# Performance work log

Measured on AMD Instinct MI355X. Metric: run time of the kernel, lower is better.

## Reference

```python
import jax, jax.numpy as jnp
import numpy as np

B, D = 4096, 512
BASE_TAU = 0.02
CLAMP_MAX = 1e36


def _l2norm(x, eps=1e-12):
    # torch F.normalize(p=2): x / max(||x||, eps)
    n = jnp.sqrt(jnp.sum(x * x, axis=-1, keepdims=True))
    return x / jnp.maximum(n, eps)


def setup_inputs() -> dict:
    key = jax.random.key(0)
    k1, k2, k3, k4, k5, k6 = jax.random.split(key, 6)
    return {
        "visual_feats": jax.random.normal(k1, (B, D), dtype=jnp.float32),
        "textual_feats": jax.random.normal(k2, (B, D), dtype=jnp.float32),
        "pid": jax.random.randint(k3, (B,), 0, 1024, dtype=jnp.int64 if jax.config.jax_enable_x64 else jnp.int32),
        "adaptive_margins": jax.random.uniform(k4, (B,), dtype=jnp.float32),
        "uncertainty_scores": jax.random.uniform(k5, (B,), dtype=jnp.float32),
        "sample_types": jax.random.randint(k6, (B,), 0, 3, dtype=jnp.int64 if jax.config.jax_enable_x64 else jnp.int32),
    }


def reference(visual_feats, textual_feats, pid, adaptive_margins, uncertainty_scores, sample_types):
    tau = BASE_TAU
    vn = _l2norm(visual_feats)
    tn = _l2norm(textual_feats)
    scores = tn @ vn.T  # [B, B]

    # Faithful to the original loop: every iteration i builds a [B,B] matrix
    # whose rows are all scores[i,:] and uses the FULL pid vector, then takes
    # row 0 of the per-sample loss. So the label/mask row is always pid[0]'s.
    labels0 = (pid == pid[0]).astype(scores.dtype)  # [B]
    mask0 = 1.0 - labels0                            # [B]
    n_neg0 = jnp.sum(mask0)

    margins = jax.lax.stop_gradient(adaptive_margins)  # .item() in torch -> no grad

    e = jnp.exp(scores / tau)  # [B, B]
    # i2t branch (row 0 of expanded matrix == scores[i,:], mask row = mask0)
    alpha = jax.lax.stop_gradient(e * labels0 / jnp.sum(e * labels0, axis=1, keepdims=True))  # [B,B]
    neg_sum = jnp.minimum(jnp.sum(e * mask0, axis=1), CLAMP_MAX)  # [B]
    loss_i2t = jnp.maximum(-jnp.sum(alpha * scores, axis=1) + tau * jnp.log(neg_sum) + margins, 0.0)

    # t2i branch: row 0 of expanded.T is scores[i,0] repeated B times;
    # alpha_t2i row 0 sums to 1 so -(alpha*s).sum == -scores[i,0].
    s0 = scores[:, 0]  # [B]
    t2i_sum = jnp.minimum(jnp.exp(s0 / tau) * n_neg0, CLAMP_MAX)
    loss_t2i = jnp.maximum(-s0 + tau * jnp.log(t2i_sum) + margins, 0.0)

    per_sample_losses = loss_i2t + loss_t2i  # [B]

    uncertain = sample_types == 2
    uncertainty_weights = jnp.where(
        uncertain,
        jnp.clip(1.0 - 0.5 * uncertainty_scores, 0.1, 1.0),
        jnp.ones_like(uncertainty_scores),
    )
    final_loss = jnp.sum(per_sample_losses * uncertainty_weights) / jnp.sum(uncertainty_weights)
    return final_loss, per_sample_losses, uncertainty_weights, scores
```

## Files before the change

### kernel.cpp

```cpp
#include <hip/hip_runtime.h>
#include <hip/hip_bf16.h>
#include <stdint.h>

#define NB 4096
#define ND 512
#define TAU_ 0.02f
#define INV_TAU_ 50.0f
#define CLAMP_MAXF 1e36f

typedef __attribute__((ext_vector_type(8))) short bf16x8;
typedef __attribute__((ext_vector_type(4))) float f32x4;

#define AS1(p) ((__attribute__((address_space(1))) void*)(uintptr_t)(p))
#define AS3(p) ((__attribute__((address_space(3))) void*)(uint32_t)(uintptr_t)(p))

static __device__ __forceinline__ unsigned short f2bf(float f) {
  __hip_bfloat16 h = __float2bfloat16(f);
  return *reinterpret_cast<unsigned short*>(&h);
}

__global__ __launch_bounds__(256) void k_norm(const float* __restrict__ vis,
                                              const float* __restrict__ txt,
                                              const int* __restrict__ pid,
                                              unsigned short* __restrict__ tn_b,
                                              unsigned short* __restrict__ vn_b,
                                              float* __restrict__ nneg) {
  if (blockIdx.x == 2048) {
    __shared__ float r4[4];
    int tid = threadIdx.x;
    int pid0 = pid[0];
    float c = 0.f;
    for (int j = tid; j < NB; j += 256) c += (pid[j] != pid0) ? 1.0f : 0.0f;
#pragma unroll
    for (int o = 32; o; o >>= 1) c += __shfl_xor(c, o, 64);
    if ((tid & 63) == 0) r4[tid >> 6] = c;
    __syncthreads();
    if (tid == 0) nneg[0] = r4[0] + r4[1] + r4[2] + r4[3];
    return;
  }
  int wv = threadIdx.x >> 6, ln = threadIdx.x & 63;
  int r = blockIdx.x * 4 + wv;
  const float* src;
  unsigned short* dst;
  if (r < NB) {
    src = txt + (size_t)r * ND;
    dst = tn_b + (size_t)r * ND;
  } else {
    src = vis + (size_t)(r - NB) * ND;
    dst = vn_b + (size_t)(r - NB) * ND;
  }
  float4 x0 = reinterpret_cast<const float4*>(src)[ln];
  float4 x1 = reinterpret_cast<const float4*>(src)[64 + ln];
  float ss = x0.x * x0.x + x0.y * x0.y + x0.z * x0.z + x0.w * x0.w +
             x1.x * x1.x + x1.y * x1.y + x1.z * x1.z + x1.w * x1.w;
#pragma unroll
  for (int o = 32; o; o >>= 1) ss += __shfl_xor(ss, o, 64);
  float inv = 1.0f / fmaxf(sqrtf(ss), 1e-12f);
  ushort4 p0, p1;
  p0.x = f2bf(x0.x * inv); p0.y = f2bf(x0.y * inv);
  p0.z = f2bf(x0.z * inv); p0.w = f2bf(x0.w * inv);
  p1.x = f2bf(x1.x * inv); p1.y = f2bf(x1.y * inv);
  p1.z = f2bf(x1.z * inv); p1.w = f2bf(x1.w * inv);
  reinterpret_cast<ushort4*>(dst)[ln] = p0;
  reinterpret_cast<ushort4*>(dst)[64 + ln] = p1;
}

__global__ __launch_bounds__(512, 2) void k_gemm(const unsigned short* __restrict__ A,
                                                 const unsigned short* __restrict__ Bm,
                                                 const int* __restrict__ pid,
                                                 float* __restrict__ C,
                                                 float* __restrict__ partials) {
  __shared__ unsigned short smem[4][2][256 * 32];
  int tid = threadIdx.x;
  int wv = tid >> 6, ln = tid & 63;
  int tile = (blockIdx.x & 7) * 32 + (blockIdx.x >> 3);
  int bm = tile >> 4;
  int bn = tile & 15;
  int wr = wv >> 2, wc = wv & 3;
  int frow = ln & 15, fkg = ln >> 4;
  f32x4 acc[8][4] = {};
  const unsigned short* Abase = A + (size_t)(bm * 256) * ND;
  const unsigned short* Bbase = Bm + (size_t)(bn * 256) * ND;

#define STAGE(bidx, k0)                                                         \
  {                                                                             \
    _Pragma("unroll") for (int p = 0; p < 2; ++p) {                             \
      int s = p * 512 + tid;                                                    \
      int rr = s >> 2;                                                          \
      int sg = ((s & 3) + (rr >> 1)) & 3;                                       \
      __builtin_amdgcn_global_load_lds(                                         \
          AS1(Abase + (size_t)rr * ND + (k0) + sg * 8),                         \
          AS3((char*)&smem[bidx][0][0] + (p * 512 + wv * 64) * 16), 16, 0, 0);  \
      __builtin_amdgcn_global_load_lds(                                         \
          AS1(Bbase + (size_t)rr * ND + (k0) + sg * 8),                         \
          AS3((char*)&smem[bidx][1][0] + (p * 512 + wv * 64) * 16), 16, 0, 0);  \
    }                                                                           \
  }

#define COMPUTE(bidx)                                                           \
  {                                                                             \
    const char* pA = (const char*)&smem[bidx][0][0];                            \
    const char* pB = (const char*)&smem[bidx][1][0];                            \
    bf16x8 af[8], bfr[4];                                                       \
    _Pragma("unroll") for (int mi = 0; mi < 8; ++mi) {                          \
      int row = wr * 128 + mi * 16 + frow;                                      \
      af[mi] = *reinterpret_cast<const bf16x8*>(                                \
          pA + row * 64 + (((fkg - (row >> 1)) & 3) * 16));                     \
    }                                                                           \
    _Pragma("unroll") for (int ni = 0; ni < 4; ++ni) {                          \
      int row = wc * 64 + ni * 16 + frow;                                       \
      bfr[ni] = *reinterpret_cast<const bf16x8*>(                               \
          pB + row * 64 + (((fkg - (row >> 1)) & 3) * 16));                     \
    }                                                                           \
    __builtin_amdgcn_s_setprio(1);                                              \
    _Pragma("unroll") for (int mi = 0; mi < 8; ++mi)                            \
      _Pragma("unroll") for (int ni = 0; ni < 4; ++ni)                          \
        acc[mi][ni] = __builtin_amdgcn_mfma_f32_16x16x32_bf16(af[mi], bfr[ni],  \
                                                              acc[mi][ni], 0, 0, 0); \
    __builtin_amdgcn_s_setprio(0);                                              \
  }

  STAGE(0, 0);
  STAGE(1, 32);
  for (int t = 0; t < 15; ++t) {
    asm volatile("s_waitcnt vmcnt(4)" ::: "memory");
    __builtin_amdgcn_s_barrier();
    if (t < 14) STAGE((t + 2) & 3, (t + 2) * 32);
    COMPUTE(t & 3);
  }
  asm volatile("s_waitcnt vmcnt(0)" ::: "memory");
  __builtin_amdgcn_s_barrier();
  COMPUTE(3);

  int pid0 = pid[0];
  int eq[4];
#pragma unroll
  for (int ni = 0; ni < 4; ++ni)
    eq[ni] = (pid[bn * 256 + wc * 64 + ni * 16 + frow] == pid0) ? 1 : 0;

  float* pb = reinterpret_cast<float*>(&smem[0][0][0]);
  float* Cp = C + (size_t)(bm * 256 + wr * 128 + fkg * 4) * NB + bn * 256 +
              wc * 64 + frow;
#pragma unroll
  for (int mi = 0; mi < 8; ++mi) {
#pragma unroll
    for (int v = 0; v < 4; ++v) {
      float sp = 0.f, sn = 0.f, sa = 0.f;
      float* rp = Cp + (size_t)(mi * 16 + v) * NB;
#pragma unroll
      for (int ni = 0; ni < 4; ++ni) {
        float s = acc[mi][ni][v];
        rp[ni * 16] = s;
        float e = __expf(s * INV_TAU_);
        if (eq[ni]) {
          sp += e;
          sa += e * s;
        } else {
          sn += e;
        }
      }
#pragma unroll
      for (int o = 1; o < 16; o <<= 1) {
        sp += __shfl_xor(sp, o, 64);
        sn += __shfl_xor(sn, o, 64);
        sa += __shfl_xor(sa, o, 64);
      }
      if (frow == 0) {
        int row = wr * 128 + mi * 16 + fkg * 4 + v;
        pb[(wc * 256 + row) * 3 + 0] = sp;
        pb[(wc * 256 + row) * 3 + 1] = sn;
        pb[(wc * 256 + row) * 3 + 2] = sa;
      }
    }
  }
  __syncthreads();
  if (tid < 256) {
    float sp = 0.f, sn = 0.f, sa = 0.f;
#pragma unroll
    for (int w = 0; w < 4; ++w) {
      sp += pb[(w * 256 + tid) * 3 + 0];
      sn += pb[(w * 256 + tid) * 3 + 1];
      sa += pb[(w * 256 + tid) * 3 + 2];
    }
    float* pout = partials + ((size_t)(bm * 256 + tid) * 16 + bn) * 3;
    pout[0] = sp;
    pout[1] = sn;
    pout[2] = sa;
  }
}

__global__ __launch_bounds__(256) void k_row2(const float* __restrict__ partials,
                                              const float* __restrict__ scores,
                                              const float* __restrict__ margins,
                                              const float* __restrict__ unc,
                                              const int* __restrict__ stypes,
                                              const float* __restrict__ nneg,
                                              float* __restrict__ psl,
                                              float* __restrict__ uw) {
  int wv = threadIdx.x >> 6, ln = threadIdx.x & 63;
  int row = blockIdx.x * 4 + wv;
  const float* p = partials + (size_t)row * 16 * 3;
  float sp = 0.f, sn = 0.f, sa = 0.f;
  if (ln < 16) {
    sp = p[ln * 3 + 0];
    sn = p[ln * 3 + 1];
    sa = p[ln * 3 + 2];
  }
#pragma unroll
  for (int o = 1; o < 16; o <<= 1) {
    sp += __shfl_xor(sp, o, 64);
    sn += __shfl_xor(sn, o, 64);
    sa += __shfl_xor(sa, o, 64);
  }
  if (ln == 0) {
    float s0v = scores[(size_t)row * NB];
    float m = margins[row];
    float li2t = fmaxf(-(sa / sp) + TAU_ * logf(fminf(sn, CLAMP_MAXF)) + m, 0.f);
    float t2i = fminf(__expf(s0v * INV_TAU_) * nneg[0], CLAMP_MAXF);
    float lt2i = fmaxf(-s0v + TAU_ * logf(t2i) + m, 0.f);
    psl[row] = li2t + lt2i;
    float w = 1.f;
    if (stypes[row] == 2) w = fminf(fmaxf(1.f - 0.5f * unc[row], 0.1f), 1.f);
    uw[row] = w;
  }
}

__global__ __launch_bounds__(256) void k_final(const float* __restrict__ psl,
                                               const float* __restrict__ uw,
                                               float* __restrict__ out) {
  __shared__ float rn[4], rd[4];
  int tid = threadIdx.x;
  float num = 0.f, den = 0.f;
  for (int j = tid; j < NB; j += 256) {
    float w = uw[j];
    num += psl[j] * w;
    den += w;
  }
#pragma unroll
  for (int o = 32; o; o >>= 1) {
    num += __shfl_xor(num, o, 64);
    den += __shfl_xor(den, o, 64);
  }
  if ((tid & 63) == 0) {
    rn[tid >> 6] = num;
    rd[tid >> 6] = den;
  }
  __syncthreads();
  if (tid == 0) {
    num = rn[0] + rn[1] + rn[2] + rn[3];
    den = rd[0] + rd[1] + rd[2] + rd[3];
    out[0] = num / den;
  }
}

extern "C" void kernel_launch(void* const* d_in, const int* in_sizes, int n_in,
                              void* d_out, int out_size, void* d_ws, size_t ws_size,
                              hipStream_t stream) {
  const float* vis = (const float*)d_in[0];
  const float* txt = (const float*)d_in[1];
  const int* pid = (const int*)d_in[2];
  const float* margins = (const float*)d_in[3];
  const float* unc = (const float*)d_in[4];
  const int* stypes = (const int*)d_in[5];

  float* out = (float*)d_out;
  float* out_psl = out + 1;
  float* out_uw = out + 1 + NB;
  float* out_scores = out + 1 + 2 * NB;

  unsigned short* tn_b = (unsigned short*)d_ws;
  unsigned short* vn_b = tn_b + (size_t)NB * ND;
  float* nneg = (float*)(vn_b + (size_t)NB * ND);
  float* partials = nneg + 4;

  k_norm<<<2049, 256, 0, stream>>>(vis, txt, pid, tn_b, vn_b, nneg);
  k_gemm<<<256, 512, 0, stream>>>(tn_b, vn_b, pid, out_scores, partials);
  k_row2<<<NB / 4, 256, 0, stream>>>(partials, out_scores, margins, unc, stypes,
                                     nneg, out_psl, out_uw);
  k_final<<<1, 256, 0, stream>>>(out_psl, out_uw, out);
}
```

Baseline: 52.14 us.

## Restructure GEMM into 256x128 tiles, two per block, with overlapped epilogue

Each block now computes two 256x128 output tiles in sequence, keeping the A panel fixed and streaming B, with a 2-stage LDS double buffer instead of the 4-stage ring. The first tile's exp/partial-sum epilogue runs in the middle of the K loop so its global stores overlap later loads. Per-wave partials now go straight to global memory without the cross-wave LDS reduction, and score column 0 is written to a side buffer so k_row2 reads it contiguously. Accumulator registers halve, which may improve latency hiding. The cost is less B reuse per tile, a barrier every K step, and four times more partial data for k_row2 to reduce.

```diff
diff --git a/kernel.cpp b/kernel.cpp
--- a/kernel.cpp
+++ b/kernel.cpp
@@ -69,41 +69,50 @@
                                                  const unsigned short* __restrict__ Bm,
                                                  const int* __restrict__ pid,
                                                  float* __restrict__ C,
-                                                 float* __restrict__ partials) {
-  __shared__ unsigned short smem[4][2][256 * 32];
+                                                 float* __restrict__ partials,
+                                                 float* __restrict__ s0g) {
+  __shared__ unsigned short smem[2][(256 + 128) * 32];
   int tid = threadIdx.x;
   int wv = tid >> 6, ln = tid & 63;
-  int tile = (blockIdx.x & 7) * 32 + (blockIdx.x >> 3);
-  int bm = tile >> 4;
-  int bn = tile & 15;
-  int wr = wv >> 2, wc = wv & 3;
+  int x = blockIdx.x & 7, i = blockIdx.x >> 3;
+  int bm = (x & 3) * 4 + (i & 3);
+  int bn0 = ((x >> 2) * 8 + (i >> 2)) * 2;
+  int wr = wv >> 1, wc = wv & 1;
   int frow = ln & 15, fkg = ln >> 4;
-  f32x4 acc[8][4] = {};
+  f32x4 acc[4][4] = {};
+  int pid0 = pid[0];
   const unsigned short* Abase = A + (size_t)(bm * 256) * ND;
-  const unsigned short* Bbase = Bm + (size_t)(bn * 256) * ND;
-
-#define STAGE(bidx, k0)                                                         \
+
+#define STAGE(bufi, tt)                                                         \
   {                                                                             \
+    int k0_ = ((tt) & 15) * 32;                                                 \
+    const unsigned short* Bb_ =                                                 \
+        Bm + (size_t)((bn0 + ((tt) >> 4)) * 128) * ND;                          \
     _Pragma("unroll") for (int p = 0; p < 2; ++p) {                             \
       int s = p * 512 + tid;                                                    \
       int rr = s >> 2;                                                          \
       int sg = ((s & 3) + (rr >> 1)) & 3;                                       \
       __builtin_amdgcn_global_load_lds(                                         \
-          AS1(Abase + (size_t)rr * ND + (k0) + sg * 8),                         \
-          AS3((char*)&smem[bidx][0][0] + (p * 512 + wv * 64) * 16), 16, 0, 0);  \
+          AS1(Abase + (size_t)rr * ND + k0_ + sg * 8),                          \
+          AS3((char*)&smem[bufi][0] + (p * 512 + wv * 64) * 16), 16, 0, 0);     \
+    }                                                                           \
+    {                                                                           \
+      int s = tid;                                                              \
+      int rr = s >> 2;                                                          \
+      int sg = ((s & 3) + (rr >> 1)) & 3;                                       \
       __builtin_amdgcn_global_load_lds(                                         \
-          AS1(Bbase + (size_t)rr * ND + (k0) + sg * 8),                         \
-          AS3((char*)&smem[bidx][1][0] + (p * 512 + wv * 64) * 16), 16, 0, 0);  \
-    }                                                                           \
-  }
-
-#define COMPUTE(bidx)                                                           \
+          AS1(Bb_ + (size_t)rr * ND + k0_ + sg * 8),                            \
+          AS3((char*)&smem[bufi][8192] + (wv * 64) * 16), 16, 0, 0);            \
+    }                                                                           \
+  }
+
+#define COMPUTE(bufi)                                                           \
   {                                                                             \
-    const char* pA = (const char*)&smem[bidx][0][0];                            \
-    const char* pB = (const char*)&smem[bidx][1][0];                            \
-    bf16x8 af[8], bfr[4];                                                       \
-    _Pragma("unroll") for (int mi = 0; mi < 8; ++mi) {                          \
-      int row = wr * 128 + mi * 16 + frow;                                      \
+    const char* pA = (const char*)&smem[bufi][0];                               \
+    const char* pB = (const char*)&smem[bufi][8192];                            \
+    bf16x8 af[4], bfr[4];                                                       \
+    _Pragma("unroll") for (int mi = 0; mi < 4; ++mi) {                          \
+      int row = wr * 64 + mi * 16 + frow;                                       \
       af[mi] = *reinterpret_cast<const bf16x8*>(                                \
           pA + row * 64 + (((fkg - (row >> 1)) & 3) * 16));                     \
     }                                                                           \
@@ -113,84 +122,64 @@
           pB + row * 64 + (((fkg - (row >> 1)) & 3) * 16));                     \
     }                                                                           \
     __builtin_amdgcn_s_setprio(1);                                              \
-    _Pragma("unroll") for (int mi = 0; mi < 8; ++mi)                            \
+    _Pragma("unroll") for (int mi = 0; mi < 4; ++mi)                            \
       _Pragma("unroll") for (int ni = 0; ni < 4; ++ni)                          \
         acc[mi][ni] = __builtin_amdgcn_mfma_f32_16x16x32_bf16(af[mi], bfr[ni],  \
                                                               acc[mi][ni], 0, 0, 0); \
     __builtin_amdgcn_s_setprio(0);                                              \
   }
 
+#define EPILOGUE(BNN)                                                           \
+  {                                                                             \
+    int eq[4];                                                                  \
+    _Pragma("unroll") for (int ni = 0; ni < 4; ++ni)                            \
+      eq[ni] = (pid[(BNN) * 128 + wc * 64 + ni * 16 + frow] == pid0) ? 1 : 0;   \
+    float* Cp = C + (size_t)(bm * 256 + wr * 64 + fkg * 4) * NB +               \
+                (BNN) * 128 + wc * 64 + frow;                                   \
+    _Pragma("unroll") for (int mi = 0; mi < 4; ++mi) {                          \
+      _Pragma("unroll") for (int v = 0; v < 4; ++v) {                           \
+        float sp = 0.f, sn = 0.f, sa = 0.f;                                     \
+        float* rp = Cp + (size_t)(mi * 16 + v) * NB;                            \
+        _Pragma("unroll") for (int ni = 0; ni < 4; ++ni) {                      \
+          float s = acc[mi][ni][v];                                             \
+          rp[ni * 16] = s;                                                      \
+          float e = __expf(s * INV_TAU_);                                       \
+          if (eq[ni]) { sp += e; sa += e * s; } else { sn += e; }               \
+        }                                                                       \
+        _Pragma("unroll") for (int o = 1; o < 16; o <<= 1) {                    \
+          sp += __shfl_xor(sp, o, 64);                                          \
+          sn += __shfl_xor(sn, o, 64);                                          \
+          sa += __shfl_xor(sa, o, 64);                                          \
+        }                                                                       \
+        if ((ln & 15) == 0) {                                                   \
+          int row = bm * 256 + wr * 64 + mi * 16 + fkg * 4 + v;                 \
+          float* po = partials + ((size_t)row * 64 + (BNN) * 2 + wc) * 3;       \
+          po[0] = sp; po[1] = sn; po[2] = sa;                                   \
+          if ((BNN) == 0 && wc == 0) s0g[row] = acc[mi][0][v];                  \
+        }                                                                       \
+      }                                                                         \
+    }                                                                           \
+  }
+
   STAGE(0, 0);
-  STAGE(1, 32);
-  for (int t = 0; t < 15; ++t) {
-    asm volatile("s_waitcnt vmcnt(4)" ::: "memory");
-    __builtin_amdgcn_s_barrier();
-    if (t < 14) STAGE((t + 2) & 3, (t + 2) * 32);
-    COMPUTE(t & 3);
-  }
-  asm volatile("s_waitcnt vmcnt(0)" ::: "memory");
-  __builtin_amdgcn_s_barrier();
-  COMPUTE(3);
-
-  int pid0 = pid[0];
-  int eq[4];
-#pragma unroll
-  for (int ni = 0; ni < 4; ++ni)
-    eq[ni] = (pid[bn * 256 + wc * 64 + ni * 16 + frow] == pid0) ? 1 : 0;
-
-  float* pb = reinterpret_cast<float*>(&smem[0][0][0]);
-  float* Cp = C + (size_t)(bm * 256 + wr * 128 + fkg * 4) * NB + bn * 256 +
-              wc * 64 + frow;
-#pragma unroll
-  for (int mi = 0; mi < 8; ++mi) {
-#pragma unroll
-    for (int v = 0; v < 4; ++v) {
-      float sp = 0.f, sn = 0.f, sa = 0.f;
-      float* rp = Cp + (size_t)(mi * 16 + v) * NB;
-#pragma unroll
-      for (int ni = 0; ni < 4; ++ni) {
-        float s = acc[mi][ni][v];
-        rp[ni * 16] = s;
-        float e = __expf(s * INV_TAU_);
-        if (eq[ni]) {
-          sp += e;
-          sa += e * s;
-        } else {
-          sn += e;
-        }
-      }
-#pragma unroll
-      for (int o = 1; o < 16; o <<= 1) {
-        sp += __shfl_xor(sp, o, 64);
-        sn += __shfl_xor(sn, o, 64);
-        sa += __shfl_xor(sa, o, 64);
-      }
-      if (frow == 0) {
-        int row = wr * 128 + mi * 16 + fkg * 4 + v;
-        pb[(wc * 256 + row) * 3 + 0] = sp;
-        pb[(wc * 256 + row) * 3 + 1] = sn;
-        pb[(wc * 256 + row) * 3 + 2] = sa;
-      }
+  __syncthreads();
+  for (int t = 0; t < 32; ++t) {
+    if (t < 31) STAGE((t + 1) & 1, t + 1);
+    COMPUTE(t & 1);
+    if (t == 15) {
+      EPILOGUE(bn0);
+#pragma unroll
+      for (int mi = 0; mi < 4; ++mi)
+#pragma unroll
+        for (int ni = 0; ni < 4; ++ni) acc[mi][ni] = (f32x4){0.f, 0.f, 0.f, 0.f};
     }
-  }
-  __syncthreads();
-  if (tid < 256) {
-    float sp = 0.f, sn = 0.f, sa = 0.f;
-#pragma unroll
-    for (int w = 0; w < 4; ++w) {
-      sp += pb[(w * 256 + tid) * 3 + 0];
-      sn += pb[(w * 256 + tid) * 3 + 1];
-      sa += pb[(w * 256 + tid) * 3 + 2];
-    }
-    float* pout = partials + ((size_t)(bm * 256 + tid) * 16 + bn) * 3;
-    pout[0] = sp;
-    pout[1] = sn;
-    pout[2] = sa;
-  }
+    __syncthreads();
+  }
+  EPILOGUE(bn0 + 1);
 }
 
 __global__ __launch_bounds__(256) void k_row2(const float* __restrict__ partials,
-                                              const float* __restrict__ scores,
+                                              const float* __restrict__ s0g,
                                               const float* __restrict__ margins,
                                               const float* __restrict__ unc,
                                               const int* __restrict__ stypes,
@@ -199,21 +188,16 @@
                                               float* __restrict__ uw) {
   int wv = threadIdx.x >> 6, ln = threadIdx.x & 63;
   int row = blockIdx.x * 4 + wv;
-  const float* p = partials + (size_t)row * 16 * 3;
-  float sp = 0.f, sn = 0.f, sa = 0.f;
-  if (ln < 16) {
-    sp = p[ln * 3 + 0];
-    sn = p[ln * 3 + 1];
-    sa = p[ln * 3 + 2];
-  }
-#pragma unroll
-  for (int o = 1; o < 16; o <<= 1) {
+  const float* p = partials + (size_t)row * 64 * 3 + ln * 3;
+  float sp = p[0], sn = p[1], sa = p[2];
+#pragma unroll
+  for (int o = 1; o < 64; o <<= 1) {
     sp += __shfl_xor(sp, o, 64);
     sn += __shfl_xor(sn, o, 64);
     sa += __shfl_xor(sa, o, 64);
   }
   if (ln == 0) {
-    float s0v = scores[(size_t)row * NB];
+    float s0v = s0g[row];
     float m = margins[row];
     float li2t = fmaxf(-(sa / sp) + TAU_ * logf(fminf(sn, CLAMP_MAXF)) + m, 0.f);
     float t2i = fminf(__expf(s0v * INV_TAU_) * nneg[0], CLAMP_MAXF);
@@ -271,11 +255,12 @@
   unsigned short* tn_b = (unsigned short*)d_ws;
   unsigned short* vn_b = tn_b + (size_t)NB * ND;
   float* nneg = (float*)(vn_b + (size_t)NB * ND);
-  float* partials = nneg + 4;
+  float* s0g = nneg + 4;
+  float* partials = s0g + NB;
 
   k_norm<<<2049, 256, 0, stream>>>(vis, txt, pid, tn_b, vn_b, nneg);
-  k_gemm<<<256, 512, 0, stream>>>(tn_b, vn_b, pid, out_scores, partials);
-  k_row2<<<NB / 4, 256, 0, stream>>>(partials, out_scores, margins, unc, stypes,
+  k_gemm<<<256, 512, 0, stream>>>(tn_b, vn_b, pid, out_scores, partials, s0g);
+  k_row2<<<NB / 4, 256, 0, stream>>>(partials, s0g, margins, unc, stypes,
                                      nneg, out_psl, out_uw);
   k_final<<<1, 256, 0, stream>>>(out_psl, out_uw, out);
 }
```

New measurement: 63.88 us. 1.23x slower.
